# Kernel optimization log

Measured on AMD Instinct MI355X. Metric: run time of the kernel, lower is better.

The kernel has to match this reference:

```python
import jax, jax.numpy as jnp
import numpy as np
from jax import lax

DN = ('NHWC', 'HWIO', 'NHWC')
NEG = -1e30  # stand-in for -inf at inactive sites during masked max-pool


def setup_inputs() -> dict:
    key = jax.random.key(0)
    ks = jax.random.split(key, 6)
    B, H, W, Cin = 1024, 21, 21, 200
    x = jax.random.normal(ks[0], (B, H, W, Cin), dtype=jnp.float32)
    mask = jax.random.randint(ks[1], (B, H, W), 0, 2, dtype=jnp.int32)
    W1 = jax.random.normal(ks[2], (2, 2, Cin, 16), dtype=jnp.float32) * 0.05
    W2 = jax.random.normal(ks[3], (5, 5, 16, 32), dtype=jnp.float32) * 0.05
    Wlin = jax.random.normal(ks[4], (32, 2), dtype=jnp.float32) * 0.1
    blin = jax.random.normal(ks[5], (2,), dtype=jnp.float32) * 0.1
    return {"x": x, "mask": mask, "W1": W1, "W2": W2, "Wlin": Wlin, "blin": blin}


def _masked_maxpool(h, m, win, stride):
    # scn.MaxPooling: max over ACTIVE sites in window; output site active iff any input active.
    hm = jnp.where(m > 0, h, NEG)
    out = lax.reduce_window(hm, NEG, lax.max, (1, win, win, 1), (1, stride, stride, 1), 'VALID')
    m_out = lax.reduce_window(m, 0.0, lax.max, (1, win, win, 1), (1, stride, stride, 1), 'VALID')
    return jnp.where(m_out > 0, out, 0.0), m_out


def reference(x, mask, W1, W2, Wlin, blin):
    m = mask.astype(x.dtype)[..., None]          # [B,21,21,1] active-site mask
    h = x * m                                    # inactive sites carry zero features
    # SubmanifoldConvolution(2, 200, 16, filter=2): size-preserving, gathers only
    # active neighbors (zeros elsewhere), outputs only at input active sites.
    h = lax.conv_general_dilated(h, W1, (1, 1), [(0, 1), (0, 1)], dimension_numbers=DN)
    h = h * m                                    # [B,21,21,16]
    # MaxPooling(2, 3, 3): 21 -> 7
    h, m = _masked_maxpool(h, m, 3, 3)
    # Convolution(2, 16, 32, filter=5, stride=1): 7 -> 3; output active iff any
    # active input in receptive field; value = sum over active inputs (== dense conv on masked feats).
    h = lax.conv_general_dilated(h, W2, (1, 1), 'VALID', dimension_numbers=DN)
    m = lax.reduce_window(m, 0.0, lax.max, (1, 5, 5, 1), (1, 1, 1, 1), 'VALID')
    h = h * m                                    # [B,3,3,32]
    # MaxPooling(2, 3, 1): 3 -> 1
    h, m = _masked_maxpool(h, m, 3, 1)           # [B,1,1,32]
    # SparseToDense already dense here; view(-1, 32), Linear(32,2), softmax(dim=1)
    h = h.reshape(-1, 32)
    return jax.nn.softmax(h @ Wlin + blin, axis=-1)   # [B,2]
```

## Files before the change

### kernel.cpp

```cpp
#include <hip/hip_runtime.h>
#include <math.h>


#define NEGINF -1e30f

__global__ __launch_bounds__(256) void conv1_pool_kernel(
    const float* __restrict__ x,
    const int*   __restrict__ mask,
    const float* __restrict__ W1,
    float* __restrict__ h2,
    float* __restrict__ m2)
{
    __shared__ float h1s[441][16];

    const int b = blockIdx.x;
    const int t = threadIdx.x;
    const int* __restrict__ mb = mask + b * 441;
    const float* __restrict__ xb = x + (size_t)b * 441 * 200;

    for (int p = t; p < 441; p += 256) {
        if (mb[p] == 0) continue;
        const int i = p / 21;
        const int j = p - i * 21;

        float acc[16];
        #pragma unroll
        for (int c = 0; c < 16; ++c) acc[c] = 0.0f;

        #pragma unroll
        for (int tap = 0; tap < 4; ++tap) {
            const int di = tap >> 1, dj = tap & 1;
            const int ii = i + di, jj = j + dj;
            if (ii < 21 && jj < 21 && mb[ii * 21 + jj] != 0) {
                const float4* __restrict__ xp =
                    (const float4*)(xb + (ii * 21 + jj) * 200);
                const float4* __restrict__ wp =
                    (const float4*)(W1 + tap * 200 * 16);

                #pragma unroll 2
                for (int k4 = 0; k4 < 50; ++k4) {
                    const float4 xv = xp[k4];
                    const float xs0 = xv.x, xs1 = xv.y, xs2 = xv.z, xs3 = xv.w;
                    #pragma unroll
                    for (int u = 0; u < 4; ++u) {
                        const float xs = (u == 0) ? xs0 : (u == 1) ? xs1 : (u == 2) ? xs2 : xs3;
                        const int k = k4 * 4 + u;
                        const float4 w0 = wp[k * 4 + 0];
                        const float4 w1 = wp[k * 4 + 1];
                        const float4 w2 = wp[k * 4 + 2];
                        const float4 w3 = wp[k * 4 + 3];
                        acc[0]  = fmaf(xs, w0.x, acc[0]);
                        acc[1]  = fmaf(xs, w0.y, acc[1]);
                        acc[2]  = fmaf(xs, w0.z, acc[2]);
                        acc[3]  = fmaf(xs, w0.w, acc[3]);
                        acc[4]  = fmaf(xs, w1.x, acc[4]);
                        acc[5]  = fmaf(xs, w1.y, acc[5]);
                        acc[6]  = fmaf(xs, w1.z, acc[6]);
                        acc[7]  = fmaf(xs, w1.w, acc[7]);
                        acc[8]  = fmaf(xs, w2.x, acc[8]);
                        acc[9]  = fmaf(xs, w2.y, acc[9]);
                        acc[10] = fmaf(xs, w2.z, acc[10]);
                        acc[11] = fmaf(xs, w2.w, acc[11]);
                        acc[12] = fmaf(xs, w3.x, acc[12]);
                        acc[13] = fmaf(xs, w3.y, acc[13]);
                        acc[14] = fmaf(xs, w3.z, acc[14]);
                        acc[15] = fmaf(xs, w3.w, acc[15]);
                    }
                }
            }
        }
        #pragma unroll
        for (int c = 0; c < 16; ++c) h1s[p][c] = acc[c];
    }

    __syncthreads();

    for (int t2 = t; t2 < 784; t2 += 256) {
        const int cell = t2 >> 4;
        const int ch   = t2 & 15;
        const int pr = cell / 7, pc = cell - pr * 7;
        float best = NEGINF;
        bool any = false;
        #pragma unroll
        for (int r = 0; r < 3; ++r) {
            #pragma unroll
            for (int c = 0; c < 3; ++c) {
                const int si = pr * 3 + r, sj = pc * 3 + c;
                if (mb[si * 21 + sj] != 0) {
                    any = true;
                    best = fmaxf(best, h1s[si * 21 + sj][ch]);
                }
            }
        }
        h2[(size_t)(b * 49 + cell) * 16 + ch] = any ? best : 0.0f;
        if (ch == 0) m2[b * 49 + cell] = any ? 1.0f : 0.0f;
    }
}

__global__ __launch_bounds__(256) void tail_kernel(
    const float* __restrict__ h2,
    const float* __restrict__ m2,
    const float* __restrict__ W2,
    const float* __restrict__ Wlin,
    const float* __restrict__ blin,
    float* __restrict__ out)
{
    __shared__ float h2s[49][16];
    __shared__ float m2s[49];
    __shared__ float hc[9][32];
    __shared__ float m3s[9];
    __shared__ float h4[32];

    const int b = blockIdx.x;
    const int t = threadIdx.x;

    for (int t2 = t; t2 < 784; t2 += 256)
        h2s[t2 >> 4][t2 & 15] = h2[(size_t)b * 784 + t2];
    if (t < 49) m2s[t] = m2[b * 49 + t];
    __syncthreads();

    for (int t2 = t; t2 < 288; t2 += 256) {
        const int cell = t2 >> 5;
        const int oc   = t2 & 31;
        const int ci = cell / 3, cj = cell - ci * 3;
        float acc = 0.0f;
        float mm = 0.0f;
        #pragma unroll
        for (int di = 0; di < 5; ++di) {
            #pragma unroll
            for (int dj = 0; dj < 5; ++dj) {
                const int s = (ci + di) * 7 + (cj + dj);
                mm = fmaxf(mm, m2s[s]);
                const float* __restrict__ wrow = W2 + ((di * 5 + dj) * 16) * 32 + oc;
                #pragma unroll
                for (int c = 0; c < 16; ++c)
                    acc = fmaf(h2s[s][c], wrow[c * 32], acc);
            }
        }
        hc[cell][oc] = (mm > 0.0f) ? acc : 0.0f;
        if (oc == 0) m3s[cell] = mm;
    }
    __syncthreads();

    if (t < 32) {
        float best = NEGINF;
        bool any = false;
        #pragma unroll
        for (int cell = 0; cell < 9; ++cell) {
            if (m3s[cell] > 0.0f) {
                any = true;
                best = fmaxf(best, hc[cell][t]);
            }
        }
        h4[t] = any ? best : 0.0f;
    }
    __syncthreads();

    if (t == 0) {
        float l0 = blin[0], l1 = blin[1];
        #pragma unroll
        for (int c = 0; c < 32; ++c) {
            l0 = fmaf(h4[c], Wlin[c * 2 + 0], l0);
            l1 = fmaf(h4[c], Wlin[c * 2 + 1], l1);
        }
        const float mx = fmaxf(l0, l1);
        const float e0 = expf(l0 - mx);
        const float e1 = expf(l1 - mx);
        const float inv = 1.0f / (e0 + e1);
        out[b * 2 + 0] = e0 * inv;
        out[b * 2 + 1] = e1 * inv;
    }
}

extern "C" void kernel_launch(void* const* d_in, const int* in_sizes, int n_in,
                              void* d_out, int out_size, void* d_ws, size_t ws_size,
                              hipStream_t stream) {
    const float* x    = (const float*)d_in[0];
    const int*   mask = (const int*)d_in[1];
    const float* W1   = (const float*)d_in[2];
    const float* W2   = (const float*)d_in[3];
    const float* Wlin = (const float*)d_in[4];
    const float* blin = (const float*)d_in[5];
    float* out = (float*)d_out;

    float* h2 = (float*)d_ws;
    float* m2 = h2 + 1024 * 49 * 16;

    conv1_pool_kernel<<<1024, 256, 0, stream>>>(x, mask, W1, h2, m2);
    tail_kernel<<<1024, 256, 0, stream>>>(h2, m2, W2, Wlin, blin, out);
}
```

Baseline: 615.8 us.

## Fuse both kernels and compute conv1 with bf16 MFMA over staged tiles

Merges the conv1+pool kernel and the tail kernel into one kernel, so the pooled features stay in shared memory and never round-trip through global memory. The 2x2 submanifold conv is recast as an implicit GEMM. Input channels are staged in chunks of 32, converted to bf16 in padded LDS, and multiplied by bf16 weights using 16x16x32 MFMA instructions. This replaces the scalar FP32 FMA loop and its redundant per-thread weight loads, at the cost of bf16 rounding of inputs and weights. It also adds more block synchronisations and a much larger LDS footprint per block.

```diff
diff --git a/kernel.cpp b/kernel.cpp
--- a/kernel.cpp
+++ b/kernel.cpp
@@ -1,143 +1,184 @@
 #include <hip/hip_runtime.h>
+#include <hip/hip_bf16.h>
 #include <math.h>
 
 
+typedef short short8 __attribute__((ext_vector_type(8)));
+typedef float f32x4 __attribute__((ext_vector_type(4)));
+
 #define NEGINF -1e30f
-
-__global__ __launch_bounds__(256) void conv1_pool_kernel(
+#define XSTR 40
+#define CELLS 506
+
+static __device__ __forceinline__ unsigned short f2bf(float f) {
+    return __builtin_bit_cast(unsigned short, __float2bfloat16(f));
+}
+
+__global__ __launch_bounds__(256) void fused_sparse_net(
     const float* __restrict__ x,
     const int*   __restrict__ mask,
     const float* __restrict__ W1,
-    float* __restrict__ h2,
-    float* __restrict__ m2)
-{
-    __shared__ float h1s[441][16];
-
-    const int b = blockIdx.x;
-    const int t = threadIdx.x;
-    const int* __restrict__ mb = mask + b * 441;
-    const float* __restrict__ xb = x + (size_t)b * 441 * 200;
-
-    for (int p = t; p < 441; p += 256) {
-        if (mb[p] == 0) continue;
-        const int i = p / 21;
-        const int j = p - i * 21;
-
-        float acc[16];
-        #pragma unroll
-        for (int c = 0; c < 16; ++c) acc[c] = 0.0f;
-
-        #pragma unroll
-        for (int tap = 0; tap < 4; ++tap) {
-            const int di = tap >> 1, dj = tap & 1;
-            const int ii = i + di, jj = j + dj;
-            if (ii < 21 && jj < 21 && mb[ii * 21 + jj] != 0) {
-                const float4* __restrict__ xp =
-                    (const float4*)(xb + (ii * 21 + jj) * 200);
-                const float4* __restrict__ wp =
-                    (const float4*)(W1 + tap * 200 * 16);
-
-                #pragma unroll 2
-                for (int k4 = 0; k4 < 50; ++k4) {
-                    const float4 xv = xp[k4];
-                    const float xs0 = xv.x, xs1 = xv.y, xs2 = xv.z, xs3 = xv.w;
-                    #pragma unroll
-                    for (int u = 0; u < 4; ++u) {
-                        const float xs = (u == 0) ? xs0 : (u == 1) ? xs1 : (u == 2) ? xs2 : xs3;
-                        const int k = k4 * 4 + u;
-                        const float4 w0 = wp[k * 4 + 0];
-                        const float4 w1 = wp[k * 4 + 1];
-                        const float4 w2 = wp[k * 4 + 2];
-                        const float4 w3 = wp[k * 4 + 3];
-                        acc[0]  = fmaf(xs, w0.x, acc[0]);
-                        acc[1]  = fmaf(xs, w0.y, acc[1]);
-                        acc[2]  = fmaf(xs, w0.z, acc[2]);
-                        acc[3]  = fmaf(xs, w0.w, acc[3]);
-                        acc[4]  = fmaf(xs, w1.x, acc[4]);
-                        acc[5]  = fmaf(xs, w1.y, acc[5]);
-                        acc[6]  = fmaf(xs, w1.z, acc[6]);
-                        acc[7]  = fmaf(xs, w1.w, acc[7]);
-                        acc[8]  = fmaf(xs, w2.x, acc[8]);
-                        acc[9]  = fmaf(xs, w2.y, acc[9]);
-                        acc[10] = fmaf(xs, w2.z, acc[10]);
-                        acc[11] = fmaf(xs, w2.w, acc[11]);
-                        acc[12] = fmaf(xs, w3.x, acc[12]);
-                        acc[13] = fmaf(xs, w3.y, acc[13]);
-                        acc[14] = fmaf(xs, w3.z, acc[14]);
-                        acc[15] = fmaf(xs, w3.w, acc[15]);
-                    }
-                }
-            }
-        }
-        #pragma unroll
-        for (int c = 0; c < 16; ++c) h1s[p][c] = acc[c];
-    }
-
-    __syncthreads();
-
-    for (int t2 = t; t2 < 784; t2 += 256) {
-        const int cell = t2 >> 4;
-        const int ch   = t2 & 15;
-        const int pr = cell / 7, pc = cell - pr * 7;
-        float best = NEGINF;
-        bool any = false;
-        #pragma unroll
-        for (int r = 0; r < 3; ++r) {
-            #pragma unroll
-            for (int c = 0; c < 3; ++c) {
-                const int si = pr * 3 + r, sj = pc * 3 + c;
-                if (mb[si * 21 + sj] != 0) {
-                    any = true;
-                    best = fmaxf(best, h1s[si * 21 + sj][ch]);
-                }
-            }
-        }
-        h2[(size_t)(b * 49 + cell) * 16 + ch] = any ? best : 0.0f;
-        if (ch == 0) m2[b * 49 + cell] = any ? 1.0f : 0.0f;
-    }
-}
-
-__global__ __launch_bounds__(256) void tail_kernel(
-    const float* __restrict__ h2,
-    const float* __restrict__ m2,
     const float* __restrict__ W2,
     const float* __restrict__ Wlin,
     const float* __restrict__ blin,
     float* __restrict__ out)
 {
+    __shared__ unsigned short xm[CELLS * XSTR];
+    __shared__ unsigned short ws[4 * 16 * XSTR];
+    __shared__ int   mb_s[441];
     __shared__ float h2s[49][16];
     __shared__ float m2s[49];
-    __shared__ float hc[9][32];
+    __shared__ float hcs[9][32];
     __shared__ float m3s[9];
-    __shared__ float h4[32];
-
-    const int b = blockIdx.x;
-    const int t = threadIdx.x;
-
-    for (int t2 = t; t2 < 784; t2 += 256)
-        h2s[t2 >> 4][t2 & 15] = h2[(size_t)b * 784 + t2];
-    if (t < 49) m2s[t] = m2[b * 49 + t];
+    __shared__ float h4s[32];
+
+    const int b    = blockIdx.x;
+    const int t    = threadIdx.x;
+    const int lane = t & 63;
+    const int wave = t >> 6;
+    const int mrow = lane & 15;
+    const int kq   = lane >> 4;
+
+    const float* __restrict__ xb = x + (size_t)b * 88200;
+    const int*   __restrict__ mb = mask + b * 441;
+
+    for (int p = t; p < 441; p += 256) mb_s[p] = mb[p];
+
+    for (int q = t; q < 172; q += 256) {
+        int pc = q >> 2, seg = q & 3;
+        int cell = (pc < 22) ? (462 + pc) : ((pc - 22) * 22 + 21);
+        short8 z = {0, 0, 0, 0, 0, 0, 0, 0};
+        *(short8*)&xm[cell * XSTR + seg * 8] = z;
+    }
+
+    int cell0[7];
+    #pragma unroll
+    for (int tile = 0; tile < 7; ++tile) {
+        int p = (wave * 7 + tile) * 16 + mrow;
+        int i = p / 21;
+        cell0[tile] = i * 22 + (p - i * 21);
+    }
+
+    f32x4 acc[7];
+    #pragma unroll
+    for (int tile = 0; tile < 7; ++tile) acc[tile] = (f32x4){0.f, 0.f, 0.f, 0.f};
+
+    for (int ch = 0; ch < 7; ++ch) {
+        __syncthreads();
+
+        for (int idx = t; idx < 2048; idx += 256) {
+            int tap = idx >> 9, rem = idx & 511;
+            int k = rem >> 4, n = rem & 15;
+            int c = ch * 32 + k;
+            float w = (c < 200) ? W1[(tap * 200 + c) * 16 + n] : 0.f;
+            ws[(tap * 16 + n) * XSTR + k] = f2bf(w);
+        }
+
+        const int niter = (ch < 6) ? 1764 : 441;
+        for (int idx = t; idx < niter; idx += 256) {
+            int pixel, seg;
+            if (ch < 6) { pixel = idx >> 2; seg = idx & 3; }
+            else        { pixel = idx;      seg = 0;       }
+            int i = pixel / 21;
+            int cell = i * 22 + (pixel - i * 21);
+            unsigned short* dst = &xm[cell * XSTR + seg * 8];
+            if (mb_s[pixel] != 0) {
+                const float4* src = (const float4*)(xb + pixel * 200 + ch * 32 + seg * 8);
+                float4 a0 = src[0];
+                float4 a1 = src[1];
+                short8 v;
+                v[0] = (short)f2bf(a0.x); v[1] = (short)f2bf(a0.y);
+                v[2] = (short)f2bf(a0.z); v[3] = (short)f2bf(a0.w);
+                v[4] = (short)f2bf(a1.x); v[5] = (short)f2bf(a1.y);
+                v[6] = (short)f2bf(a1.z); v[7] = (short)f2bf(a1.w);
+                *(short8*)dst = v;
+            } else {
+                short8 z = {0, 0, 0, 0, 0, 0, 0, 0};
+                *(short8*)dst = z;
+            }
+        }
+        __syncthreads();
+
+        short8 bfrag[4];
+        #pragma unroll
+        for (int tap = 0; tap < 4; ++tap)
+            bfrag[tap] = *(const short8*)&ws[(tap * 16 + mrow) * XSTR + kq * 8];
+
+        #pragma unroll
+        for (int tile = 0; tile < 7; ++tile) {
+            #pragma unroll
+            for (int tap = 0; tap < 4; ++tap) {
+                int cell = cell0[tile] + (tap >> 1) * 22 + (tap & 1);
+                short8 afrag = *(const short8*)&xm[cell * XSTR + kq * 8];
+                acc[tile] = __builtin_amdgcn_mfma_f32_16x16x32_bf16(
+                    afrag, bfrag[tap], acc[tile], 0, 0, 0);
+            }
+        }
+    }
+
+    __syncthreads();
+
+    float (*h1s)[17] = (float (*)[17])(void*)xm;
+    #pragma unroll
+    for (int tile = 0; tile < 7; ++tile) {
+        #pragma unroll
+        for (int r = 0; r < 4; ++r) {
+            int p = (wave * 7 + tile) * 16 + kq * 4 + r;
+            if (p < 441) h1s[p][mrow] = acc[tile][r];
+        }
+    }
+    __syncthreads();
+
+    for (int t2 = t; t2 < 784; t2 += 256) {
+        int cell = t2 >> 4, c = t2 & 15;
+        int pr = cell / 7, pc = cell - pr * 7;
+        float best = NEGINF;
+        bool any = false;
+        #pragma unroll
+        for (int r = 0; r < 3; ++r) {
+            #pragma unroll
+            for (int cc = 0; cc < 3; ++cc) {
+                int s = (pr * 3 + r) * 21 + (pc * 3 + cc);
+                if (mb_s[s] != 0) { any = true; best = fmaxf(best, h1s[s][c]); }
+            }
+        }
+        h2s[cell][c] = any ? best : 0.0f;
+        if (c == 0) m2s[cell] = any ? 1.0f : 0.0f;
+    }
     __syncthreads();
 
     for (int t2 = t; t2 < 288; t2 += 256) {
-        const int cell = t2 >> 5;
-        const int oc   = t2 & 31;
-        const int ci = cell / 3, cj = cell - ci * 3;
-        float acc = 0.0f;
-        float mm = 0.0f;
+        int cell = t2 >> 5, oc = t2 & 31;
+        int ci = cell / 3, cj = cell - ci * 3;
+        float a2 = 0.f, mm = 0.f;
         #pragma unroll
         for (int di = 0; di < 5; ++di) {
             #pragma unroll
             for (int dj = 0; dj < 5; ++dj) {
-                const int s = (ci + di) * 7 + (cj + dj);
+                int s = (ci + di) * 7 + (cj + dj);
                 mm = fmaxf(mm, m2s[s]);
-                const float* __restrict__ wrow = W2 + ((di * 5 + dj) * 16) * 32 + oc;
-                #pragma unroll
-                for (int c = 0; c < 16; ++c)
-                    acc = fmaf(h2s[s][c], wrow[c * 32], acc);
-            }
-        }
-        hc[cell][oc] = (mm > 0.0f) ? acc : 0.0f;
+                const float* __restrict__ wp2 = W2 + ((di * 5 + dj) * 16) * 32 + oc;
+                const float4* hv = (const float4*)&h2s[s][0];
+                float4 h0 = hv[0], h1v = hv[1], h2v = hv[2], h3v = hv[3];
+                a2 = fmaf(h0.x,  wp2[0 * 32],  a2);
+                a2 = fmaf(h0.y,  wp2[1 * 32],  a2);
+                a2 = fmaf(h0.z,  wp2[2 * 32],  a2);
+                a2 = fmaf(h0.w,  wp2[3 * 32],  a2);
+                a2 = fmaf(h1v.x, wp2[4 * 32],  a2);
+                a2 = fmaf(h1v.y, wp2[5 * 32],  a2);
+                a2 = fmaf(h1v.z, wp2[6 * 32],  a2);
+                a2 = fmaf(h1v.w, wp2[7 * 32],  a2);
+                a2 = fmaf(h2v.x, wp2[8 * 32],  a2);
+                a2 = fmaf(h2v.y, wp2[9 * 32],  a2);
+                a2 = fmaf(h2v.z, wp2[10 * 32], a2);
+                a2 = fmaf(h2v.w, wp2[11 * 32], a2);
+                a2 = fmaf(h3v.x, wp2[12 * 32], a2);
+                a2 = fmaf(h3v.y, wp2[13 * 32], a2);
+                a2 = fmaf(h3v.z, wp2[14 * 32], a2);
+                a2 = fmaf(h3v.w, wp2[15 * 32], a2);
+            }
+        }
+        hcs[cell][oc] = (mm > 0.f) ? a2 : 0.f;
         if (oc == 0) m3s[cell] = mm;
     }
     __syncthreads();
@@ -147,12 +188,9 @@
         bool any = false;
         #pragma unroll
         for (int cell = 0; cell < 9; ++cell) {
-            if (m3s[cell] > 0.0f) {
-                any = true;
-                best = fmaxf(best, hc[cell][t]);
-            }
-        }
-        h4[t] = any ? best : 0.0f;
+            if (m3s[cell] > 0.f) { any = true; best = fmaxf(best, hcs[cell][t]); }
+        }
+        h4s[t] = any ? best : 0.f;
     }
     __syncthreads();
 
@@ -160,13 +198,13 @@
         float l0 = blin[0], l1 = blin[1];
         #pragma unroll
         for (int c = 0; c < 32; ++c) {
-            l0 = fmaf(h4[c], Wlin[c * 2 + 0], l0);
-            l1 = fmaf(h4[c], Wlin[c * 2 + 1], l1);
-        }
-        const float mx = fmaxf(l0, l1);
-        const float e0 = expf(l0 - mx);
-        const float e1 = expf(l1 - mx);
-        const float inv = 1.0f / (e0 + e1);
+            l0 = fmaf(h4s[c], Wlin[c * 2 + 0], l0);
+            l1 = fmaf(h4s[c], Wlin[c * 2 + 1], l1);
+        }
+        float mx = fmaxf(l0, l1);
+        float e0 = expf(l0 - mx);
+        float e1 = expf(l1 - mx);
+        float inv = 1.f / (e0 + e1);
         out[b * 2 + 0] = e0 * inv;
         out[b * 2 + 1] = e1 * inv;
     }
@@ -183,9 +221,5 @@
     const float* blin = (const float*)d_in[5];
     float* out = (float*)d_out;
 
-    float* h2 = (float*)d_ws;
-    float* m2 = h2 + 1024 * 49 * 16;
-
-    conv1_pool_kernel<<<1024, 256, 0, stream>>>(x, mask, W1, h2, m2);
-    tail_kernel<<<1024, 256, 0, stream>>>(h2, m2, W2, Wlin, blin, out);
+    fused_sparse_net<<<1024, 256, 0, stream>>>(x, mask, W1, W2, Wlin, blin, out);
 }
```

Measured after the change: 647.9 us. +5.2%, slower.
